# Kernel optimization log

Measured on AMD Instinct MI355X. Metric: run time of the kernel, lower is better.

Reference implementation:

```python
import jax, jax.numpy as jnp
import numpy as np

N = 100000      # nodes
E = 1600000     # directed edges (avg degree 16)
D_IN, D_H, D_OUT = 128, 128, 1


def gcn_conv(x, src, dst, W, b, n):
    """PyG GCNConv: out = D^{-1/2} (A+I) D^{-1/2} X W + b.
    src/dst already include self-loops. deg counted on dst (in-degree)."""
    h = x @ W                                            # [n, d_out]
    deg = jax.ops.segment_sum(jnp.ones(src.shape[0], h.dtype), dst, num_segments=n)
    dinv = jax.lax.rsqrt(jnp.maximum(deg, 1.0))          # deg >= 1 (self loops)
    norm = dinv[src] * dinv[dst]                         # [e]
    msg = h[src] * norm[:, None]                         # gather + scale, [e, d_out]
    out = jax.ops.segment_sum(msg, dst, num_segments=n)  # scatter-add, [n, d_out]
    return out + b


def setup_inputs() -> dict:
    key = jax.random.key(0)
    ks = jax.random.split(key, 8)
    x = jax.random.normal(ks[0], (N, D_IN), dtype=jnp.float32)
    edge_index = jax.random.randint(ks[1], (2, E), 0, N, dtype=jnp.int64)

    def glorot(k, fan_in, fan_out):
        s = jnp.sqrt(6.0 / (fan_in + fan_out)).astype(jnp.float32)
        return jax.random.uniform(k, (fan_in, fan_out), jnp.float32, -s, s)

    W0 = glorot(ks[2], D_IN, D_H)
    b0 = jnp.zeros((D_H,), jnp.float32)
    W1 = glorot(ks[3], D_H, D_H)
    b1 = jnp.zeros((D_H,), jnp.float32)
    W2 = glorot(ks[4], D_H, D_OUT)
    b2 = jnp.zeros((D_OUT,), jnp.float32)
    return {"x": x, "edge_index": edge_index,
            "W0": W0, "b0": b0, "W1": W1, "b1": b1, "W2": W2, "b2": b2}


def reference(x, edge_index, W0, b0, W1, b1, W2, b2):
    n = x.shape[0]
    loops = jnp.arange(n, dtype=edge_index.dtype)
    src = jnp.concatenate([edge_index[0], loops])
    dst = jnp.concatenate([edge_index[1], loops])
    # dropout is identity in eval mode
    h = jax.nn.relu(gcn_conv(x, src, dst, W0, b0, n))
    h = jax.nn.relu(gcn_conv(h, src, dst, W1, b1, n))
    out = gcn_conv(h, src, dst, W2, b2, n)
    return jax.nn.sigmoid(out)
```

## Files before the change

kernel.cpp:

```cpp
#include <hip/hip_runtime.h>
#include <cstddef>

#define D 128
#define BW_LOG 11
#define BW 2048
#define CHUNK 8192
#define GP 136
typedef unsigned int uint;
typedef unsigned short ushort;

typedef __attribute__((ext_vector_type(8))) short bf16x8;
typedef __attribute__((ext_vector_type(4))) float f32x4;

static __device__ __forceinline__ uint bf16r(float x) {
  uint u = __float_as_uint(x);
  return (u + 0x7fffu + ((u >> 16) & 1u)) >> 16;
}
static __device__ __forceinline__ uint pack2(float a, float b) {
  return bf16r(a) | (bf16r(b) << 16);
}
static __device__ __forceinline__ void acc_bf16x8(const uint4 v, float* a) {
  a[0] += __uint_as_float(v.x << 16);
  a[1] += __uint_as_float(v.x & 0xffff0000u);
  a[2] += __uint_as_float(v.y << 16);
  a[3] += __uint_as_float(v.y & 0xffff0000u);
  a[4] += __uint_as_float(v.z << 16);
  a[5] += __uint_as_float(v.z & 0xffff0000u);
  a[6] += __uint_as_float(v.w << 16);
  a[7] += __uint_as_float(v.w & 0xffff0000u);
}

__global__ void k_bzero(int* __restrict__ bcnt, int nb) {
  int t = threadIdx.x;
  if (t < nb) bcnt[t] = 0;
}

__global__ __launch_bounds__(512)
void k_bhist(const int* __restrict__ dstA, int* __restrict__ bcnt, int e, int nb) {
  __shared__ int h[256];
  int t = threadIdx.x;
  if (t < nb) h[t] = 0;
  __syncthreads();
  int base = blockIdx.x * CHUNK;
  int m = min(CHUNK, e - base);
  for (int i = t; i < m; i += 512) atomicAdd(&h[dstA[base + i] >> BW_LOG], 1);
  __syncthreads();
  if (t < nb && h[t]) atomicAdd(&bcnt[t], h[t]);
}

__global__ void k_bscan(const int* __restrict__ bcnt, int* __restrict__ bbase,
                        int* __restrict__ cursor, int* __restrict__ off,
                        int nb, int n, int e) {
  __shared__ int s[256];
  int t = threadIdx.x;
  int v = (t < nb) ? bcnt[t] : 0;
  s[t] = v;
  __syncthreads();
  for (int d = 1; d < 256; d <<= 1) {
    int x = (t >= d) ? s[t - d] : 0;
    __syncthreads();
    s[t] += x;
    __syncthreads();
  }
  if (t < nb) {
    int b = s[t] - v;
    bbase[t] = b;
    cursor[t] = b;
  }
  if (t == 0) {
    bbase[nb] = e;
    off[n] = e;
  }
}

__global__ __launch_bounds__(512)
void k_bscatter(const int* __restrict__ ei, int* __restrict__ cursor,
                int* __restrict__ pk, int e, int nb) {
  __shared__ int h[256], lbase[256], gpos[256], lcur[256], s2[256];
  __shared__ int staged[CHUNK];
  int t = threadIdx.x;
  if (t < nb) h[t] = 0;
  __syncthreads();
  int base = blockIdx.x * CHUNK;
  int m = min(CHUNK, e - base);
  int sv[16], dv[16];
#pragma unroll
  for (int k = 0; k < 16; ++k) {
    int i = t + k * 512;
    sv[k] = 0; dv[k] = 0;
    if (i < m) {
      sv[k] = ei[base + i];
      dv[k] = ei[e + base + i];
      atomicAdd(&h[dv[k] >> BW_LOG], 1);
    }
  }
  __syncthreads();
  if (t < 256) s2[t] = (t < nb) ? h[t] : 0;
  __syncthreads();
  for (int d = 1; d < 256; d <<= 1) {
    int x = 0;
    if (t < 256 && t >= d) x = s2[t - d];
    __syncthreads();
    if (t < 256) s2[t] += x;
    __syncthreads();
  }
  if (t < nb) {
    lbase[t] = s2[t] - h[t];
    lcur[t] = s2[t] - h[t];
    gpos[t] = h[t] ? atomicAdd(&cursor[t], h[t]) : 0;
  }
  __syncthreads();
#pragma unroll
  for (int k = 0; k < 16; ++k) {
    int i = t + k * 512;
    if (i < m) {
      int b = dv[k] >> BW_LOG;
      int p = atomicAdd(&lcur[b], 1);
      staged[p] = sv[k] | ((dv[k] & (BW - 1)) << 17);
    }
  }
  __syncthreads();
  for (int b = 0; b < nb; ++b) {
    int cnt = h[b], lb = lbase[b], gp = gpos[b];
    for (int i = t; i < cnt; i += 512) pk[gp + i] = staged[lb + i];
  }
}

__global__ __launch_bounds__(1024)
void k_bfinal(const int* __restrict__ bbase, const int* __restrict__ pk,
              int* __restrict__ off, float* __restrict__ dinv,
              int* __restrict__ csr, int n, int nb) {
  __shared__ int sc[BW];
  __shared__ int lcur[BW];
  const int b = blockIdx.x;
  const int t = threadIdx.x;
  const int e0 = bbase[b], e1 = bbase[b + 1];
  const int node0 = b << BW_LOG;
  sc[t] = 0; sc[t + 1024] = 0;
  lcur[t] = 0; lcur[t + 1024] = 0;
  __syncthreads();
  for (int i = e0 + t; i < e1; i += 1024) atomicAdd(&sc[(pk[i] >> 17) & (BW - 1)], 1);
  __syncthreads();
  int c0 = sc[t], c1 = sc[t + 1024];
  for (int d = 1; d < BW; d <<= 1) {
    int v0 = (t >= d) ? sc[t - d] : 0;
    int v1 = (t + 1024 >= d) ? sc[t + 1024 - d] : 0;
    __syncthreads();
    sc[t] += v0; sc[t + 1024] += v1;
    __syncthreads();
  }
  int ex0 = sc[t] - c0, ex1 = sc[t + 1024] - c1;
  int na = node0 + t, nbn = node0 + t + 1024;
  if (na < n)  { off[na]  = e0 + ex0; dinv[na]  = rsqrtf((float)c0 + 1.0f); }
  if (nbn < n) { off[nbn] = e0 + ex1; dinv[nbn] = rsqrtf((float)c1 + 1.0f); }
  __syncthreads();
  sc[t] = ex0; sc[t + 1024] = ex1;
  __syncthreads();
  for (int i = e0 + t; i < e1; i += 1024) {
    int v = pk[i];
    int dl = (v >> 17) & (BW - 1);
    int p = atomicAdd(&lcur[dl], 1);
    csr[e0 + sc[dl] + p] = v & 0x1FFFF;
  }
}

__global__ void k_wsplit(const float* __restrict__ W0, const float* __restrict__ W1,
                         ushort* __restrict__ out) {
  int idx = blockIdx.x * 256 + threadIdx.x;
  if (idx >= 32768) return;
  int lay = idx >> 14;
  int rem = idx & 16383;
  int col = rem >> 7, k = rem & 127;
  const float* W = lay ? W1 : W0;
  float w = W[k * D + col];
  uint hb = bf16r(w);
  float hf = __uint_as_float(hb << 16);
  out[lay * 32768 + rem] = (ushort)hb;
  out[lay * 32768 + 16384 + rem] = (ushort)bf16r(w - hf);
}

template <bool BF16A>
__global__ __launch_bounds__(256)
void k_mgemm(const void* __restrict__ Xv, const ushort* __restrict__ Wht,
             const ushort* __restrict__ Wlt, const float* __restrict__ dinv,
             ushort* __restrict__ Asb, int n, int nstrips) {
  __shared__ __align__(16) ushort Wh[128 * GP];
  const int tid = threadIdx.x;

  for (int c = tid; c < 2048; c += 256) {
    *(uint4*)(&Wh[(c >> 4) * GP + (c & 15) * 8]) = *(const uint4*)(Wht + c * 8);
  }
  __syncthreads();

  const int wv = tid >> 6;
  const int l = tid & 63;
  const int lr = l & 15;
  const int lk = (l >> 4) * 8;

  const float* Xf = (const float*)Xv;
  const ushort* Xb = (const ushort*)Xv;

  for (int strip = blockIdx.x * 4 + wv; strip < nstrips; strip += gridDim.x * 4) {
    const int row0 = strip * 16;
    f32x4 acc[8];
#pragma unroll
    for (int t = 0; t < 8; ++t) acc[t] = (f32x4){0.f, 0.f, 0.f, 0.f};

    const int arow = row0 + lr;
    const bool av = (arow < n);

#pragma unroll
    for (int ks = 0; ks < 4; ++ks) {
      const int k0 = ks * 32 + lk;
      bf16x8 ahv, alv;
      if (BF16A) {
        if (av) {
          ahv = *(const bf16x8*)(Xb + (size_t)arow * D + k0);
        } else {
          union { bf16x8 v; ushort a[8]; } z;
#pragma unroll
          for (int j = 0; j < 8; ++j) z.a[j] = 0;
          ahv = z.v;
        }
      } else {
        float a8[8];
        if (av) {
          const float* ap = Xf + (size_t)arow * D + k0;
          float4 u0 = *(const float4*)(ap);
          float4 u1 = *(const float4*)(ap + 4);
          a8[0] = u0.x; a8[1] = u0.y; a8[2] = u0.z; a8[3] = u0.w;
          a8[4] = u1.x; a8[5] = u1.y; a8[6] = u1.z; a8[7] = u1.w;
        } else {
#pragma unroll
          for (int j = 0; j < 8; ++j) a8[j] = 0.f;
        }
        union { bf16x8 v; ushort a[8]; } ah, al;
#pragma unroll
        for (int j = 0; j < 8; ++j) {
          uint hb = bf16r(a8[j]);
          float hf = __uint_as_float(hb << 16);
          ah.a[j] = (ushort)hb;
          al.a[j] = (ushort)bf16r(a8[j] - hf);
        }
        ahv = ah.v;
        alv = al.v;
      }
#pragma unroll
      for (int nt = 0; nt < 8; ++nt) {
        bf16x8 bh = *(const bf16x8*)(&Wh[(nt * 16 + lr) * GP + k0]);
        bf16x8 bl = *(const bf16x8*)(Wlt + (size_t)(nt * 16 + lr) * D + k0);
        acc[nt] = __builtin_amdgcn_mfma_f32_16x16x32_bf16(ahv, bh, acc[nt], 0, 0, 0);
        if (!BF16A)
          acc[nt] = __builtin_amdgcn_mfma_f32_16x16x32_bf16(alv, bh, acc[nt], 0, 0, 0);
        acc[nt] = __builtin_amdgcn_mfma_f32_16x16x32_bf16(ahv, bl, acc[nt], 0, 0, 0);
      }
    }

#pragma unroll
    for (int r = 0; r < 4; ++r) {
      int row = row0 + (l >> 4) * 4 + r;
      if (row < n) {
        float di = dinv[row];
#pragma unroll
        for (int nt = 0; nt < 8; ++nt) {
          Asb[(size_t)row * D + nt * 16 + lr] = (ushort)bf16r(acc[nt][r] * di);
        }
      }
    }
  }
}

template <bool FUSE_DOT>
__global__ __launch_bounds__(256)
void k_gather(const int* __restrict__ off, const int* __restrict__ csr,
              const float* __restrict__ dinv, const ushort* __restrict__ Asb,
              ushort* __restrict__ Bb, const float* __restrict__ bias,
              const float* __restrict__ W2, float* __restrict__ ss, int n) {
  const int wid = blockIdx.x * 4 + (threadIdx.x >> 6);
  if (wid >= n) return;
  const int lane = threadIdx.x & 63;
  const int q = lane >> 4;
  const int li = lane & 15;
  const int c = li << 3;

  float a[8];
#pragma unroll
  for (int k = 0; k < 8; ++k) a[k] = 0.f;
  if (q == 0) {
    uint4 sv = *(const uint4*)(Asb + (size_t)wid * D + c);
    acc_bf16x8(sv, a);
  }

  const int o0 = off[wid], o1 = off[wid + 1];
  for (int j0 = o0; j0 < o1; j0 += 64) {
    int sj = 0;
    if (j0 + lane < o1) sj = csr[j0 + lane];
    const int m = min(64, o1 - j0);
    const int nst = (m + 3) >> 2;
#pragma unroll 4
    for (int t = 0; t < nst; ++t) {
      int idx = (t << 2) + q;
      int s = __shfl(sj, idx);
      if (idx < m) {
        uint4 v = *(const uint4*)(Asb + (size_t)s * D + c);
        acc_bf16x8(v, a);
      }
    }
  }

#pragma unroll
  for (int k = 0; k < 8; ++k) {
    a[k] += __shfl_xor(a[k], 16);
    a[k] += __shfl_xor(a[k], 32);
  }

  const float di = dinv[wid];
  float4 bb0 = *(const float4*)(bias + c);
  float4 bb1 = *(const float4*)(bias + c + 4);
  float v0 = fmaxf(a[0] * di + bb0.x, 0.f);
  float v1 = fmaxf(a[1] * di + bb0.y, 0.f);
  float v2 = fmaxf(a[2] * di + bb0.z, 0.f);
  float v3 = fmaxf(a[3] * di + bb0.w, 0.f);
  float v4 = fmaxf(a[4] * di + bb1.x, 0.f);
  float v5 = fmaxf(a[5] * di + bb1.y, 0.f);
  float v6 = fmaxf(a[6] * di + bb1.z, 0.f);
  float v7 = fmaxf(a[7] * di + bb1.w, 0.f);

  if (FUSE_DOT) {
    float4 w0 = *(const float4*)(W2 + c);
    float4 w1 = *(const float4*)(W2 + c + 4);
    float p = v0 * w0.x + v1 * w0.y + v2 * w0.z + v3 * w0.w +
              v4 * w1.x + v5 * w1.y + v6 * w1.z + v7 * w1.w;
    p += __shfl_xor(p, 1);
    p += __shfl_xor(p, 2);
    p += __shfl_xor(p, 4);
    p += __shfl_xor(p, 8);
    if (lane == 0) ss[wid] = p * di;
  } else {
    if (lane < 16) {
      uint4 w;
      w.x = pack2(v0, v1);
      w.y = pack2(v2, v3);
      w.z = pack2(v4, v5);
      w.w = pack2(v6, v7);
      *(uint4*)(Bb + (size_t)wid * D + c) = w;
    }
  }
}

__global__ void k_gather_scalar(const int* __restrict__ off, const int* __restrict__ csr,
                                const float* __restrict__ dinv, const float* __restrict__ ss,
                                const float* __restrict__ b2, float* __restrict__ out, int n) {
  int i = blockIdx.x * 256 + threadIdx.x;
  if (i >= n) return;
  float acc = ss[i];
  int j = off[i], o1 = off[i + 1];
  float a0 = 0.f, a1 = 0.f, a2 = 0.f, a3 = 0.f;
  for (; j + 4 <= o1; j += 4) {
    int s0 = csr[j], s1 = csr[j + 1], s2 = csr[j + 2], s3 = csr[j + 3];
    a0 += ss[s0];
    a1 += ss[s1];
    a2 += ss[s2];
    a3 += ss[s3];
  }
  for (; j < o1; ++j) a0 += ss[csr[j]];
  acc += (a0 + a1) + (a2 + a3);
  float v = acc * dinv[i] + b2[0];
  out[i] = 1.f / (1.f + expf(-v));
}

extern "C" void kernel_launch(void* const* d_in, const int* in_sizes, int n_in,
                              void* d_out, int out_size, void* d_ws, size_t ws_size,
                              hipStream_t stream) {
  const float* x  = (const float*)d_in[0];
  const int*   ei = (const int*)d_in[1];
  const float* W0 = (const float*)d_in[2];
  const float* b0 = (const float*)d_in[3];
  const float* W1 = (const float*)d_in[4];
  const float* b1 = (const float*)d_in[5];
  const float* W2 = (const float*)d_in[6];
  const float* b2 = (const float*)d_in[7];
  float* out = (float*)d_out;

  const int n = in_sizes[0] / D;
  const int e = in_sizes[1] / 2;
  const int nb = (n + BW - 1) / BW;
  const int nstrips = (n + 15) / 16;
  const size_t np = ((size_t)n + 256) / 256 * 256;

  float* ws = (float*)d_ws;
  int*    off    = (int*)ws;
  float*  dinv   = ws + np;
  float*  ss     = ws + 2 * np;
  int*    bmeta  = (int*)(ws + 3 * np);
  int*    bcnt   = bmeta;
  int*    bbase  = bmeta + 260;
  int*    cursor = bmeta + 600;
  ushort* wsp    = (ushort*)(ws + 3 * np + 1024);
  int*    csr    = (int*)(ws + 3 * np + 1024 + 32768);
  int*    pk     = csr + e;
  ushort* Asb    = (ushort*)(pk + e);
  ushort* Bb     = Asb + (size_t)n * D;

  const ushort* W0h = wsp;
  const ushort* W0l = wsp + 16384;
  const ushort* W1h = wsp + 32768;
  const ushort* W1l = wsp + 49152;

  const int g256n = (n + 255) / 256;
  const int ggath = (n + 3) / 4;
  const int gchnk = (e + CHUNK - 1) / CHUNK;
  const int ggemm = (nstrips + 3) / 4 < 1024 ? (nstrips + 3) / 4 : 1024;

  k_wsplit<<<128, 256, 0, stream>>>(W0, W1, (ushort*)wsp);
  k_bzero<<<1, 256, 0, stream>>>(bcnt, nb);
  k_bhist<<<gchnk, 512, 0, stream>>>(ei + e, bcnt, e, nb);
  k_bscan<<<1, 256, 0, stream>>>(bcnt, bbase, cursor, off, nb, n, e);
  k_bscatter<<<gchnk, 512, 0, stream>>>(ei, cursor, pk, e, nb);
  k_bfinal<<<nb, 1024, 0, stream>>>(bbase, pk, off, dinv, csr, n, nb);

  k_mgemm<false><<<ggemm, 256, 0, stream>>>(x, W0h, W0l, dinv, Asb, n, nstrips);
  k_gather<false><<<ggath, 256, 0, stream>>>(off, csr, dinv, Asb, Bb, b0, nullptr, nullptr, n);

  k_mgemm<true><<<ggemm, 256, 0, stream>>>(Bb, W1h, W1l, dinv, Asb, n, nstrips);
  k_gather<true><<<ggath, 256, 0, stream>>>(off, csr, dinv, Asb, nullptr, b1, W2, ss, n);

  k_gather_scalar<<<g256n, 256, 0, stream>>>(off, csr, dinv, ss, b2, out, n);
}
```

Before: 295.5 us.

## Fuse layer-1 aggregation with layer-2 GEMM and shrink CSR bucket width

The layer-1 neighbor gather is fused with the layer-2 MFMA GEMM. Each block gathers 16 nodes into an LDS tile, applies bias and ReLU, then multiplies by W1 before writing the scaled result. This removes the intermediate Bb round trip through global memory and one kernel launch. The CSR bucket width also drops from 2048 to 512 nodes, giving more, smaller k_bfinal blocks with less scan work each. The risks are a grid capped at 1024 blocks with per-group barriers, lower gather parallelism per block, and idle threads in the bucket scan.

```diff
diff --git a/kernel.cpp b/kernel.cpp
--- a/kernel.cpp
+++ b/kernel.cpp
@@ -2,8 +2,8 @@
 #include <cstddef>
 
 #define D 128
-#define BW_LOG 11
-#define BW 2048
+#define BW_LOG 9
+#define BW 512
 #define CHUNK 8192
 #define GP 136
 typedef unsigned int uint;
@@ -136,25 +136,25 @@
   const int t = threadIdx.x;
   const int e0 = bbase[b], e1 = bbase[b + 1];
   const int node0 = b << BW_LOG;
-  sc[t] = 0; sc[t + 1024] = 0;
-  lcur[t] = 0; lcur[t + 1024] = 0;
+  if (t < BW) { sc[t] = 0; lcur[t] = 0; }
   __syncthreads();
   for (int i = e0 + t; i < e1; i += 1024) atomicAdd(&sc[(pk[i] >> 17) & (BW - 1)], 1);
   __syncthreads();
-  int c0 = sc[t], c1 = sc[t + 1024];
+  int c0 = (t < BW) ? sc[t] : 0;
   for (int d = 1; d < BW; d <<= 1) {
-    int v0 = (t >= d) ? sc[t - d] : 0;
-    int v1 = (t + 1024 >= d) ? sc[t + 1024 - d] : 0;
-    __syncthreads();
-    sc[t] += v0; sc[t + 1024] += v1;
-    __syncthreads();
-  }
-  int ex0 = sc[t] - c0, ex1 = sc[t + 1024] - c1;
-  int na = node0 + t, nbn = node0 + t + 1024;
-  if (na < n)  { off[na]  = e0 + ex0; dinv[na]  = rsqrtf((float)c0 + 1.0f); }
-  if (nbn < n) { off[nbn] = e0 + ex1; dinv[nbn] = rsqrtf((float)c1 + 1.0f); }
-  __syncthreads();
-  sc[t] = ex0; sc[t + 1024] = ex1;
+    int v0 = (t < BW && t >= d) ? sc[t - d] : 0;
+    __syncthreads();
+    if (t < BW) sc[t] += v0;
+    __syncthreads();
+  }
+  if (t < BW) {
+    int na = node0 + t;
+    if (na < n) {
+      off[na] = e0 + sc[t] - c0;
+      dinv[na] = rsqrtf((float)c0 + 1.0f);
+    }
+    sc[t] -= c0;
+  }
   __syncthreads();
   for (int i = e0 + t; i < e1; i += 1024) {
     int v = pk[i];
@@ -179,17 +179,15 @@
   out[lay * 32768 + 16384 + rem] = (ushort)bf16r(w - hf);
 }
 
-template <bool BF16A>
 __global__ __launch_bounds__(256)
-void k_mgemm(const void* __restrict__ Xv, const ushort* __restrict__ Wht,
-             const ushort* __restrict__ Wlt, const float* __restrict__ dinv,
-             ushort* __restrict__ Asb, int n, int nstrips) {
+void k_mgemm0(const float* __restrict__ Xf, const ushort* __restrict__ Wht,
+              const ushort* __restrict__ Wlt, const float* __restrict__ dinv,
+              ushort* __restrict__ Asb, int n, int nstrips) {
   __shared__ __align__(16) ushort Wh[128 * GP];
   const int tid = threadIdx.x;
 
-  for (int c = tid; c < 2048; c += 256) {
+  for (int c = tid; c < 2048; c += 256)
     *(uint4*)(&Wh[(c >> 4) * GP + (c & 15) * 8]) = *(const uint4*)(Wht + c * 8);
-  }
   __syncthreads();
 
   const int wv = tid >> 6;
@@ -197,9 +195,6 @@
   const int lr = l & 15;
   const int lk = (l >> 4) * 8;
 
-  const float* Xf = (const float*)Xv;
-  const ushort* Xb = (const ushort*)Xv;
-
   for (int strip = blockIdx.x * 4 + wv; strip < nstrips; strip += gridDim.x * 4) {
     const int row0 = strip * 16;
     f32x4 acc[8];
@@ -212,47 +207,32 @@
 #pragma unroll
     for (int ks = 0; ks < 4; ++ks) {
       const int k0 = ks * 32 + lk;
-      bf16x8 ahv, alv;
-      if (BF16A) {
-        if (av) {
-          ahv = *(const bf16x8*)(Xb + (size_t)arow * D + k0);
-        } else {
-          union { bf16x8 v; ushort a[8]; } z;
-#pragma unroll
-          for (int j = 0; j < 8; ++j) z.a[j] = 0;
-          ahv = z.v;
-        }
+      float a8[8];
+      if (av) {
+        const float* ap = Xf + (size_t)arow * D + k0;
+        float4 u0 = *(const float4*)(ap);
+        float4 u1 = *(const float4*)(ap + 4);
+        a8[0] = u0.x; a8[1] = u0.y; a8[2] = u0.z; a8[3] = u0.w;
+        a8[4] = u1.x; a8[5] = u1.y; a8[6] = u1.z; a8[7] = u1.w;
       } else {
-        float a8[8];
-        if (av) {
-          const float* ap = Xf + (size_t)arow * D + k0;
-          float4 u0 = *(const float4*)(ap);
-          float4 u1 = *(const float4*)(ap + 4);
-          a8[0] = u0.x; a8[1] = u0.y; a8[2] = u0.z; a8[3] = u0.w;
-          a8[4] = u1.x; a8[5] = u1.y; a8[6] = u1.z; a8[7] = u1.w;
-        } else {
-#pragma unroll
-          for (int j = 0; j < 8; ++j) a8[j] = 0.f;
-        }
-        union { bf16x8 v; ushort a[8]; } ah, al;
-#pragma unroll
-        for (int j = 0; j < 8; ++j) {
-          uint hb = bf16r(a8[j]);
-          float hf = __uint_as_float(hb << 16);
-          ah.a[j] = (ushort)hb;
-          al.a[j] = (ushort)bf16r(a8[j] - hf);
-        }
-        ahv = ah.v;
-        alv = al.v;
+#pragma unroll
+        for (int j = 0; j < 8; ++j) a8[j] = 0.f;
+      }
+      union { bf16x8 v; ushort a[8]; } ah, al;
+#pragma unroll
+      for (int j = 0; j < 8; ++j) {
+        uint hb = bf16r(a8[j]);
+        float hf = __uint_as_float(hb << 16);
+        ah.a[j] = (ushort)hb;
+        al.a[j] = (ushort)bf16r(a8[j] - hf);
       }
 #pragma unroll
       for (int nt = 0; nt < 8; ++nt) {
         bf16x8 bh = *(const bf16x8*)(&Wh[(nt * 16 + lr) * GP + k0]);
         bf16x8 bl = *(const bf16x8*)(Wlt + (size_t)(nt * 16 + lr) * D + k0);
-        acc[nt] = __builtin_amdgcn_mfma_f32_16x16x32_bf16(ahv, bh, acc[nt], 0, 0, 0);
-        if (!BF16A)
-          acc[nt] = __builtin_amdgcn_mfma_f32_16x16x32_bf16(alv, bh, acc[nt], 0, 0, 0);
-        acc[nt] = __builtin_amdgcn_mfma_f32_16x16x32_bf16(ahv, bl, acc[nt], 0, 0, 0);
+        acc[nt] = __builtin_amdgcn_mfma_f32_16x16x32_bf16(ah.v, bh, acc[nt], 0, 0, 0);
+        acc[nt] = __builtin_amdgcn_mfma_f32_16x16x32_bf16(al.v, bh, acc[nt], 0, 0, 0);
+        acc[nt] = __builtin_amdgcn_mfma_f32_16x16x32_bf16(ah.v, bl, acc[nt], 0, 0, 0);
       }
     }
 
@@ -270,12 +250,120 @@
   }
 }
 
-template <bool FUSE_DOT>
 __global__ __launch_bounds__(256)
-void k_gather(const int* __restrict__ off, const int* __restrict__ csr,
-              const float* __restrict__ dinv, const ushort* __restrict__ Asb,
-              ushort* __restrict__ Bb, const float* __restrict__ bias,
-              const float* __restrict__ W2, float* __restrict__ ss, int n) {
+void k_gather_gemm(const int* __restrict__ off, const int* __restrict__ csr,
+                   const float* __restrict__ dinv, const ushort* __restrict__ Asb0,
+                   const ushort* __restrict__ Wht, const ushort* __restrict__ Wlt,
+                   const float* __restrict__ bias, ushort* __restrict__ Asb1,
+                   int n, int ngroups) {
+  __shared__ __align__(16) ushort Wh[128 * GP];
+  __shared__ __align__(16) ushort tile[16 * GP];
+  const int tid = threadIdx.x;
+
+  for (int c = tid; c < 2048; c += 256)
+    *(uint4*)(&Wh[(c >> 4) * GP + (c & 15) * 8]) = *(const uint4*)(Wht + c * 8);
+
+  const int wv = tid >> 6;
+  const int l = tid & 63;
+  const int q = l >> 4;
+  const int li = l & 15;
+  const int c8 = li << 3;
+
+  for (int g = blockIdx.x; g < ngroups; g += gridDim.x) {
+    const int node0 = g << 4;
+
+    for (int s = 0; s < 4; ++s) {
+      const int wid = node0 + wv * 4 + s;
+      float a[8];
+#pragma unroll
+      for (int k = 0; k < 8; ++k) a[k] = 0.f;
+      if (wid < n) {
+        if (q == 0) {
+          uint4 sv = *(const uint4*)(Asb0 + (size_t)wid * D + c8);
+          acc_bf16x8(sv, a);
+        }
+        const int o0 = off[wid], o1 = off[wid + 1];
+        for (int j0 = o0; j0 < o1; j0 += 64) {
+          int sj = 0;
+          if (j0 + l < o1) sj = csr[j0 + l];
+          const int m = min(64, o1 - j0);
+          const int nst = (m + 3) >> 2;
+#pragma unroll 4
+          for (int t = 0; t < nst; ++t) {
+            int idx = (t << 2) + q;
+            int sn = __shfl(sj, idx);
+            if (idx < m) {
+              uint4 v = *(const uint4*)(Asb0 + (size_t)sn * D + c8);
+              acc_bf16x8(v, a);
+            }
+          }
+        }
+#pragma unroll
+        for (int k = 0; k < 8; ++k) {
+          a[k] += __shfl_xor(a[k], 16);
+          a[k] += __shfl_xor(a[k], 32);
+        }
+      }
+      if (l < 16) {
+        uint4 w = make_uint4(0u, 0u, 0u, 0u);
+        if (wid < n) {
+          const float di = dinv[wid];
+          float4 bb0 = *(const float4*)(bias + c8);
+          float4 bb1 = *(const float4*)(bias + c8 + 4);
+          float v0 = fmaxf(a[0] * di + bb0.x, 0.f);
+          float v1 = fmaxf(a[1] * di + bb0.y, 0.f);
+          float v2 = fmaxf(a[2] * di + bb0.z, 0.f);
+          float v3 = fmaxf(a[3] * di + bb0.w, 0.f);
+          float v4 = fmaxf(a[4] * di + bb1.x, 0.f);
+          float v5 = fmaxf(a[5] * di + bb1.y, 0.f);
+          float v6 = fmaxf(a[6] * di + bb1.z, 0.f);
+          float v7 = fmaxf(a[7] * di + bb1.w, 0.f);
+          w.x = pack2(v0, v1);
+          w.y = pack2(v2, v3);
+          w.z = pack2(v4, v5);
+          w.w = pack2(v6, v7);
+        }
+        *(uint4*)(&tile[(wv * 4 + s) * GP + c8]) = w;
+      }
+    }
+    __syncthreads();
+
+    const int lr = li;
+    const int lk = q << 3;
+    const int nt0 = wv * 2;
+    f32x4 acc0 = (f32x4){0.f, 0.f, 0.f, 0.f};
+    f32x4 acc1 = (f32x4){0.f, 0.f, 0.f, 0.f};
+#pragma unroll
+    for (int ks = 0; ks < 4; ++ks) {
+      const int k0 = ks * 32 + lk;
+      bf16x8 ah = *(const bf16x8*)(&tile[lr * GP + k0]);
+      bf16x8 bh0 = *(const bf16x8*)(&Wh[(nt0 * 16 + lr) * GP + k0]);
+      bf16x8 bl0 = *(const bf16x8*)(Wlt + (size_t)(nt0 * 16 + lr) * D + k0);
+      bf16x8 bh1 = *(const bf16x8*)(&Wh[((nt0 + 1) * 16 + lr) * GP + k0]);
+      bf16x8 bl1 = *(const bf16x8*)(Wlt + (size_t)((nt0 + 1) * 16 + lr) * D + k0);
+      acc0 = __builtin_amdgcn_mfma_f32_16x16x32_bf16(ah, bh0, acc0, 0, 0, 0);
+      acc0 = __builtin_amdgcn_mfma_f32_16x16x32_bf16(ah, bl0, acc0, 0, 0, 0);
+      acc1 = __builtin_amdgcn_mfma_f32_16x16x32_bf16(ah, bh1, acc1, 0, 0, 0);
+      acc1 = __builtin_amdgcn_mfma_f32_16x16x32_bf16(ah, bl1, acc1, 0, 0, 0);
+    }
+#pragma unroll
+    for (int r = 0; r < 4; ++r) {
+      int row = node0 + q * 4 + r;
+      if (row < n) {
+        float di = dinv[row];
+        Asb1[(size_t)row * D + nt0 * 16 + lr] = (ushort)bf16r(acc0[r] * di);
+        Asb1[(size_t)row * D + (nt0 + 1) * 16 + lr] = (ushort)bf16r(acc1[r] * di);
+      }
+    }
+    __syncthreads();
+  }
+}
+
+__global__ __launch_bounds__(256)
+void k_gather_dot(const int* __restrict__ off, const int* __restrict__ csr,
+                  const float* __restrict__ dinv, const ushort* __restrict__ Asb,
+                  const float* __restrict__ bias, const float* __restrict__ W2,
+                  float* __restrict__ ss, int n) {
   const int wid = blockIdx.x * 4 + (threadIdx.x >> 6);
   if (wid >= n) return;
   const int lane = threadIdx.x & 63;
@@ -317,35 +405,21 @@
   const float di = dinv[wid];
   float4 bb0 = *(const float4*)(bias + c);
   float4 bb1 = *(const float4*)(bias + c + 4);
-  float v0 = fmaxf(a[0] * di + bb0.x, 0.f);
-  float v1 = fmaxf(a[1] * di + bb0.y, 0.f);
-  float v2 = fmaxf(a[2] * di + bb0.z, 0.f);
-  float v3 = fmaxf(a[3] * di + bb0.w, 0.f);
-  float v4 = fmaxf(a[4] * di + bb1.x, 0.f);
-  float v5 = fmaxf(a[5] * di + bb1.y, 0.f);
-  float v6 = fmaxf(a[6] * di + bb1.z, 0.f);
-  float v7 = fmaxf(a[7] * di + bb1.w, 0.f);
-
-  if (FUSE_DOT) {
-    float4 w0 = *(const float4*)(W2 + c);
-    float4 w1 = *(const float4*)(W2 + c + 4);
-    float p = v0 * w0.x + v1 * w0.y + v2 * w0.z + v3 * w0.w +
-              v4 * w1.x + v5 * w1.y + v6 * w1.z + v7 * w1.w;
-    p += __shfl_xor(p, 1);
-    p += __shfl_xor(p, 2);
-    p += __shfl_xor(p, 4);
-    p += __shfl_xor(p, 8);
-    if (lane == 0) ss[wid] = p * di;
-  } else {
-    if (lane < 16) {
-      uint4 w;
-      w.x = pack2(v0, v1);
-      w.y = pack2(v2, v3);
-      w.z = pack2(v4, v5);
-      w.w = pack2(v6, v7);
-      *(uint4*)(Bb + (size_t)wid * D + c) = w;
-    }
-  }
+  float4 w0 = *(const float4*)(W2 + c);
+  float4 w1 = *(const float4*)(W2 + c + 4);
+  float p = fmaxf(a[0] * di + bb0.x, 0.f) * w0.x +
+            fmaxf(a[1] * di + bb0.y, 0.f) * w0.y +
+            fmaxf(a[2] * di + bb0.z, 0.f) * w0.z +
+            fmaxf(a[3] * di + bb0.w, 0.f) * w0.w +
+            fmaxf(a[4] * di + bb1.x, 0.f) * w1.x +
+            fmaxf(a[5] * di + bb1.y, 0.f) * w1.y +
+            fmaxf(a[6] * di + bb1.z, 0.f) * w1.z +
+            fmaxf(a[7] * di + bb1.w, 0.f) * w1.w;
+  p += __shfl_xor(p, 1);
+  p += __shfl_xor(p, 2);
+  p += __shfl_xor(p, 4);
+  p += __shfl_xor(p, 8);
+  if (lane == 0) ss[wid] = p * di;
 }
 
 __global__ void k_gather_scalar(const int* __restrict__ off, const int* __restrict__ csr,
@@ -386,6 +460,7 @@
   const int e = in_sizes[1] / 2;
   const int nb = (n + BW - 1) / BW;
   const int nstrips = (n + 15) / 16;
+  const int ngroups = nstrips;
   const size_t np = ((size_t)n + 256) / 256 * 256;
 
   float* ws = (float*)d_ws;
@@ -399,8 +474,8 @@
   ushort* wsp    = (ushort*)(ws + 3 * np + 1024);
   int*    csr    = (int*)(ws + 3 * np + 1024 + 32768);
   int*    pk     = csr + e;
-  ushort* Asb    = (ushort*)(pk + e);
-  ushort* Bb     = Asb + (size_t)n * D;
+  ushort* Asb0   = (ushort*)(pk + e);
+  ushort* Asb1   = Asb0 + (size_t)n * D;
 
   const ushort* W0h = wsp;
   const ushort* W0l = wsp + 16384;
@@ -411,6 +486,7 @@
   const int ggath = (n + 3) / 4;
   const int gchnk = (e + CHUNK - 1) / CHUNK;
   const int ggemm = (nstrips + 3) / 4 < 1024 ? (nstrips + 3) / 4 : 1024;
+  const int gfuse = ngroups < 1024 ? ngroups : 1024;
 
   k_wsplit<<<128, 256, 0, stream>>>(W0, W1, (ushort*)wsp);
   k_bzero<<<1, 256, 0, stream>>>(bcnt, nb);
@@ -419,11 +495,11 @@
   k_bscatter<<<gchnk, 512, 0, stream>>>(ei, cursor, pk, e, nb);
   k_bfinal<<<nb, 1024, 0, stream>>>(bbase, pk, off, dinv, csr, n, nb);
 
-  k_mgemm<false><<<ggemm, 256, 0, stream>>>(x, W0h, W0l, dinv, Asb, n, nstrips);
-  k_gather<false><<<ggath, 256, 0, stream>>>(off, csr, dinv, Asb, Bb, b0, nullptr, nullptr, n);
-
-  k_mgemm<true><<<ggemm, 256, 0, stream>>>(Bb, W1h, W1l, dinv, Asb, n, nstrips);
-  k_gather<true><<<ggath, 256, 0, stream>>>(off, csr, dinv, Asb, nullptr, b1, W2, ss, n);
+  k_mgemm0<<<ggemm, 256, 0, stream>>>(x, W0h, W0l, dinv, Asb0, n, nstrips);
+
+  k_gather_gemm<<<gfuse, 256, 0, stream>>>(off, csr, dinv, Asb0, W1h, W1l, b0, Asb1, n, ngroups);
+
+  k_gather_dot<<<ggath, 256, 0, stream>>>(off, csr, dinv, Asb1, b1, W2, ss, n);
 
   k_gather_scalar<<<g256n, 256, 0, stream>>>(off, csr, dinv, ss, b2, out, n);
 }
```

New measurement: 317.5 us. +7.4%, slower.

## Shrink CSR buckets, parallelize bucket scatter copy, use packed f32x2 accumulation

Applied to the files above, without the earlier changes.

Reduces the dst bucket width from 2048 to 512 nodes, so the bucketing kernels produce more buckets and k_bfinal launches more, smaller blocks. The per-bucket serial copy loop in k_bscatter becomes a flat parallel loop that finds each element's bucket by binary search over the local prefix sums. The gather kernel accumulates bf16 values into f32x2 vectors, so the compiler can emit packed FP32 adds. Risks include many more k_bfinal blocks each using only half their threads, plus extra binary-search work per element; the bucket count must also stay within 256 so it fits the shared histogram.

```diff
diff --git a/kernel.cpp b/kernel.cpp
--- a/kernel.cpp
+++ b/kernel.cpp
@@ -2,8 +2,8 @@
 #include <cstddef>
 
 #define D 128
-#define BW_LOG 11
-#define BW 2048
+#define BW_LOG 9
+#define BW 512
 #define CHUNK 8192
 #define GP 136
 typedef unsigned int uint;
@@ -11,6 +11,7 @@
 
 typedef __attribute__((ext_vector_type(8))) short bf16x8;
 typedef __attribute__((ext_vector_type(4))) float f32x4;
+typedef __attribute__((ext_vector_type(2))) float f32x2;
 
 static __device__ __forceinline__ uint bf16r(float x) {
   uint u = __float_as_uint(x);
@@ -19,15 +20,17 @@
 static __device__ __forceinline__ uint pack2(float a, float b) {
   return bf16r(a) | (bf16r(b) << 16);
 }
-static __device__ __forceinline__ void acc_bf16x8(const uint4 v, float* a) {
-  a[0] += __uint_as_float(v.x << 16);
-  a[1] += __uint_as_float(v.x & 0xffff0000u);
-  a[2] += __uint_as_float(v.y << 16);
-  a[3] += __uint_as_float(v.y & 0xffff0000u);
-  a[4] += __uint_as_float(v.z << 16);
-  a[5] += __uint_as_float(v.z & 0xffff0000u);
-  a[6] += __uint_as_float(v.w << 16);
-  a[7] += __uint_as_float(v.w & 0xffff0000u);
+static __device__ __forceinline__ void accp(uint w, f32x2* a) {
+  f32x2 t;
+  t.x = __uint_as_float(w << 16);
+  t.y = __uint_as_float(w & 0xffff0000u);
+  *a += t;
+}
+static __device__ __forceinline__ void acc_bf16x8p(const uint4 v, f32x2* a) {
+  accp(v.x, a + 0);
+  accp(v.y, a + 1);
+  accp(v.z, a + 2);
+  accp(v.w, a + 3);
 }
 
 __global__ void k_bzero(int* __restrict__ bcnt, int nb) {
@@ -39,7 +42,7 @@
 void k_bhist(const int* __restrict__ dstA, int* __restrict__ bcnt, int e, int nb) {
   __shared__ int h[256];
   int t = threadIdx.x;
-  if (t < nb) h[t] = 0;
+  if (t < 256) h[t] = 0;
   __syncthreads();
   int base = blockIdx.x * CHUNK;
   int m = min(CHUNK, e - base);
@@ -76,10 +79,10 @@
 __global__ __launch_bounds__(512)
 void k_bscatter(const int* __restrict__ ei, int* __restrict__ cursor,
                 int* __restrict__ pk, int e, int nb) {
-  __shared__ int h[256], lbase[256], gpos[256], lcur[256], s2[256];
+  __shared__ int h[256], s2[256], gpos[256], lcur[256];
   __shared__ int staged[CHUNK];
   int t = threadIdx.x;
-  if (t < nb) h[t] = 0;
+  if (t < 256) h[t] = 0;
   __syncthreads();
   int base = blockIdx.x * CHUNK;
   int m = min(CHUNK, e - base);
@@ -95,7 +98,7 @@
     }
   }
   __syncthreads();
-  if (t < 256) s2[t] = (t < nb) ? h[t] : 0;
+  if (t < 256) s2[t] = h[t];
   __syncthreads();
   for (int d = 1; d < 256; d <<= 1) {
     int x = 0;
@@ -104,10 +107,9 @@
     if (t < 256) s2[t] += x;
     __syncthreads();
   }
-  if (t < nb) {
-    lbase[t] = s2[t] - h[t];
+  if (t < 256) {
     lcur[t] = s2[t] - h[t];
-    gpos[t] = h[t] ? atomicAdd(&cursor[t], h[t]) : 0;
+    gpos[t] = (t < nb && h[t]) ? atomicAdd(&cursor[t], h[t]) : 0;
   }
   __syncthreads();
 #pragma unroll
@@ -120,9 +122,14 @@
     }
   }
   __syncthreads();
-  for (int b = 0; b < nb; ++b) {
-    int cnt = h[b], lb = lbase[b], gp = gpos[b];
-    for (int i = t; i < cnt; i += 512) pk[gp + i] = staged[lb + i];
+  for (int i = t; i < m; i += 512) {
+    int lo = 0, hi = nb;
+    while (lo < hi) {
+      int mid = (lo + hi) >> 1;
+      if (s2[mid] <= i) lo = mid + 1; else hi = mid;
+    }
+    int lb = s2[lo] - h[lo];
+    pk[gpos[lo] + (i - lb)] = staged[i];
   }
 }
 
@@ -136,25 +143,25 @@
   const int t = threadIdx.x;
   const int e0 = bbase[b], e1 = bbase[b + 1];
   const int node0 = b << BW_LOG;
-  sc[t] = 0; sc[t + 1024] = 0;
-  lcur[t] = 0; lcur[t + 1024] = 0;
+  if (t < BW) { sc[t] = 0; lcur[t] = 0; }
   __syncthreads();
   for (int i = e0 + t; i < e1; i += 1024) atomicAdd(&sc[(pk[i] >> 17) & (BW - 1)], 1);
   __syncthreads();
-  int c0 = sc[t], c1 = sc[t + 1024];
+  int c0 = (t < BW) ? sc[t] : 0;
   for (int d = 1; d < BW; d <<= 1) {
-    int v0 = (t >= d) ? sc[t - d] : 0;
-    int v1 = (t + 1024 >= d) ? sc[t + 1024 - d] : 0;
-    __syncthreads();
-    sc[t] += v0; sc[t + 1024] += v1;
-    __syncthreads();
-  }
-  int ex0 = sc[t] - c0, ex1 = sc[t + 1024] - c1;
-  int na = node0 + t, nbn = node0 + t + 1024;
-  if (na < n)  { off[na]  = e0 + ex0; dinv[na]  = rsqrtf((float)c0 + 1.0f); }
-  if (nbn < n) { off[nbn] = e0 + ex1; dinv[nbn] = rsqrtf((float)c1 + 1.0f); }
-  __syncthreads();
-  sc[t] = ex0; sc[t + 1024] = ex1;
+    int v0 = (t < BW && t >= d) ? sc[t - d] : 0;
+    __syncthreads();
+    if (t < BW) sc[t] += v0;
+    __syncthreads();
+  }
+  if (t < BW) {
+    int na = node0 + t;
+    if (na < n) {
+      off[na] = e0 + sc[t] - c0;
+      dinv[na] = rsqrtf((float)c0 + 1.0f);
+    }
+    sc[t] -= c0;
+  }
   __syncthreads();
   for (int i = e0 + t; i < e1; i += 1024) {
     int v = pk[i];
@@ -187,9 +194,8 @@
   __shared__ __align__(16) ushort Wh[128 * GP];
   const int tid = threadIdx.x;
 
-  for (int c = tid; c < 2048; c += 256) {
+  for (int c = tid; c < 2048; c += 256)
     *(uint4*)(&Wh[(c >> 4) * GP + (c & 15) * 8]) = *(const uint4*)(Wht + c * 8);
-  }
   __syncthreads();
 
   const int wv = tid >> 6;
@@ -283,12 +289,12 @@
   const int li = lane & 15;
   const int c = li << 3;
 
-  float a[8];
-#pragma unroll
-  for (int k = 0; k < 8; ++k) a[k] = 0.f;
+  f32x2 a2[4];
+#pragma unroll
+  for (int k = 0; k < 4; ++k) a2[k] = (f32x2){0.f, 0.f};
   if (q == 0) {
     uint4 sv = *(const uint4*)(Asb + (size_t)wid * D + c);
-    acc_bf16x8(sv, a);
+    acc_bf16x8p(sv, a2);
   }
 
   const int o0 = off[wid], o1 = off[wid + 1];
@@ -303,11 +309,14 @@
       int s = __shfl(sj, idx);
       if (idx < m) {
         uint4 v = *(const uint4*)(Asb + (size_t)s * D + c);
-        acc_bf16x8(v, a);
+        acc_bf16x8p(v, a2);
       }
     }
   }
 
+  float a[8];
+#pragma unroll
+  for (int k = 0; k < 4; ++k) { a[2 * k] = a2[k].x; a[2 * k + 1] = a2[k].y; }
 #pragma unroll
   for (int k = 0; k < 8; ++k) {
     a[k] += __shfl_xor(a[k], 16);
```

Measured after the change: 281.0 us. 4.9% less time.
